# Kernel optimization log

Measured on AMD Instinct MI355X. Metric: run time of the kernel, lower is better.

Reference implementation:

```python
import jax, jax.numpy as jnp
import numpy as np

N = 100000      # nodes
E = 1600000     # edges (avg degree 16)
IN_DIM = 64
H = 4           # num_heads
D = 32          # out_dim per head
NEG_SLOPE = 0.1


def setup_inputs() -> dict:
    key = jax.random.key(0)
    k_x, k_src, k_dst, k_w, k_fc, k_al, k_ar = jax.random.split(key, 7)
    x = jax.random.normal(k_x, (N, IN_DIM), dtype=jnp.float32)
    src = jax.random.randint(k_src, (E,), 0, N, dtype=jnp.int32)
    dst = jax.random.randint(k_dst, (E,), 0, N, dtype=jnp.int32)
    w = jax.random.uniform(k_w, (E,), dtype=jnp.float32)
    # xavier-ish init for learned params
    W_fc = jax.random.normal(k_fc, (IN_DIM, H * D), dtype=jnp.float32) * (2.0 / (IN_DIM + H * D)) ** 0.5
    attn_l = jax.random.normal(k_al, (1, H, D), dtype=jnp.float32) * 0.1
    attn_r = jax.random.normal(k_ar, (1, H, D), dtype=jnp.float32) * 0.1
    vt = jnp.zeros((1,), dtype=jnp.float32)  # unused by forward (as in the source)
    return {"vt": vt, "x": x, "src": src, "dst": dst, "w": w,
            "W_fc": W_fc, "attn_l": attn_l, "attn_r": attn_r}


def reference(vt, x, src, dst, w, W_fc, attn_l, attn_r):
    # node projection: [N, H, D]
    feat = (x @ W_fc).reshape(-1, H, D)
    el = jnp.sum(feat * attn_l, axis=-1)  # [N, H]
    er = jnp.sum(feat * attn_r, axis=-1)  # [N, H]
    # per-edge logits: u_add_v then leaky_relu, scaled by edge weight w
    e = el[src] + er[dst]                                   # [E, H]
    e = jnp.where(e >= 0, e, NEG_SLOPE * e)                 # leaky_relu
    e = w[:, None] * e                                      # [E, H]
    # edge softmax grouped by destination node (numerically stable)
    m = jax.ops.segment_max(e, dst, num_segments=N)         # [N, H]
    ex = jnp.exp(e - m[dst])                                # [E, H]
    den = jax.ops.segment_sum(ex, dst, num_segments=N)      # [N, H]
    a = ex / den[dst]                                       # [E, H]
    # message passing: u_mul_e -> sum over incoming edges
    msg = feat[src] * a[:, :, None]                         # [E, H, D]
    out = jax.ops.segment_sum(msg, dst, num_segments=N)     # [N, H, D]
    return out
```

## Files before the change

### kernel.cpp

```cpp
#include <hip/hip_runtime.h>
#include <math.h>

#define IN_DIM 64
#define HH 4
#define CC 128
#define NEG_SLOPE 0.1f

typedef __attribute__((ext_vector_type(8))) short short8;
typedef __attribute__((ext_vector_type(4))) float f32x4;

__device__ __forceinline__ float leaky(float v) { return v >= 0.f ? v : NEG_SLOPE * v; }

__device__ __forceinline__ unsigned f2bf(float f) {
  unsigned u = __float_as_uint(f);
  unsigned r = u + 0x7FFFu + ((u >> 16) & 1u);
  return r >> 16;
}

__global__ void k_prepw(const float* __restrict__ W, unsigned* __restrict__ wt) {
  int tid = blockIdx.x * 256 + threadIdx.x;
  if (tid >= 128 * 32) return;
  int n = tid >> 5;
  int r = tid & 31;
  int b = r >> 2, h = r & 3;
  int k = b * 8 + h * 2;
  unsigned lo = f2bf(W[k * CC + n]);
  unsigned hi = f2bf(W[(k + 1) * CC + n]);
  wt[n * 32 + (b ^ (n & 7)) * 4 + h] = lo | (hi << 16);
}

__global__ __launch_bounds__(256) void k_project(
    const float* __restrict__ x, const unsigned* __restrict__ wt,
    const float* __restrict__ attn_l, const float* __restrict__ attn_r,
    unsigned char* __restrict__ featQ, float* __restrict__ scale,
    float* __restrict__ el, float* __restrict__ er, int N)
{
  __shared__ unsigned Wlds[4096];
  __shared__ float Al[CC], Ar[CC];
  int t = threadIdx.x;
  {
    const uint4* s = (const uint4*)wt;
    uint4* d = (uint4*)Wlds;
#pragma unroll
    for (int i = 0; i < 4; ++i) d[t + 256 * i] = s[t + 256 * i];
  }
  if (t < CC) { Al[t] = attn_l[t]; Ar[t] = attn_r[t]; }
  __syncthreads();

  int lane = t & 63;
  int l4 = lane >> 4, l16 = lane & 15;
  int node = blockIdx.x * 64 + (t >> 6) * 16 + l16;
  bool valid = node < N;
  int nrow = valid ? node : 0;

  short8 bfr[2];
#pragma unroll
  for (int s = 0; s < 2; ++s) {
    const float4* xp = (const float4*)&x[(size_t)nrow * 64 + s * 32 + l4 * 8];
    float4 xa = xp[0], xb = xp[1];
    union { short8 v; unsigned u[4]; } pk;
    pk.u[0] = f2bf(xa.x) | (f2bf(xa.y) << 16);
    pk.u[1] = f2bf(xa.z) | (f2bf(xa.w) << 16);
    pk.u[2] = f2bf(xb.x) | (f2bf(xb.y) << 16);
    pk.u[3] = f2bf(xb.z) | (f2bf(xb.w) << 16);
    bfr[s] = pk.v;
  }

  f32x4 acc[8];
#pragma unroll
  for (int c = 0; c < 8; ++c) acc[c] = (f32x4){0.f, 0.f, 0.f, 0.f};

#pragma unroll
  for (int c = 0; c < 8; ++c) {
    int n0 = c * 16 + l16;
    int sw = n0 & 7;
#pragma unroll
    for (int s = 0; s < 2; ++s) {
      int b = s * 4 + l4;
      union { short8 v; uint4 q; } af;
      af.q = *(const uint4*)&Wlds[n0 * 32 + (b ^ sw) * 4];
      acc[c] = __builtin_amdgcn_mfma_f32_16x16x32_bf16(af.v, bfr[s], acc[c], 0, 0, 0);
    }
  }

  float mx = 0.f;
#pragma unroll
  for (int c = 0; c < 8; ++c) {
#pragma unroll
    for (int r = 0; r < 4; ++r) mx = fmaxf(mx, fabsf(acc[c][r]));
  }
  mx = fmaxf(mx, __shfl_xor(mx, 16, 64));
  mx = fmaxf(mx, __shfl_xor(mx, 32, 64));
  float mxs = fmaxf(mx, 1e-20f);
  float inv = 127.f / mxs;

  if (valid) {
#pragma unroll
    for (int c = 0; c < 8; ++c) {
      int q0 = __float2int_rn(acc[c][0] * inv) + 128;
      int q1 = __float2int_rn(acc[c][1] * inv) + 128;
      int q2 = __float2int_rn(acc[c][2] * inv) + 128;
      int q3 = __float2int_rn(acc[c][3] * inv) + 128;
      unsigned u = (unsigned)(q0 & 0xff) | ((unsigned)(q1 & 0xff) << 8) |
                   ((unsigned)(q2 & 0xff) << 16) | ((unsigned)(q3 & 0xff) << 24);
      *(unsigned*)&featQ[(size_t)node * 128 + c * 16 + l4 * 4] = u;
    }
    if (l4 == 0) scale[node] = mxs * (1.f / 127.f);
  }

  float pl[4], pr[4];
#pragma unroll
  for (int h = 0; h < 4; ++h) {
    float sl = 0.f, sr = 0.f;
#pragma unroll
    for (int ct = 0; ct < 2; ++ct) {
      int c = 2 * h + ct;
      int cb = c * 16 + l4 * 4;
#pragma unroll
      for (int r = 0; r < 4; ++r) {
        sl = fmaf(acc[c][r], Al[cb + r], sl);
        sr = fmaf(acc[c][r], Ar[cb + r], sr);
      }
    }
    sl += __shfl_xor(sl, 16, 64); sl += __shfl_xor(sl, 32, 64);
    sr += __shfl_xor(sr, 16, 64); sr += __shfl_xor(sr, 32, 64);
    pl[h] = sl; pr[h] = sr;
  }
  if (l4 == 0 && valid) {
    *(float4*)&el[(size_t)node * 4] = make_float4(pl[0], pl[1], pl[2], pl[3]);
    *(float4*)&er[(size_t)node * 4] = make_float4(pr[0], pr[1], pr[2], pr[3]);
  }
}

__global__ __launch_bounds__(256) void k_bhist(const int* __restrict__ dst,
                                               int* __restrict__ bcnt, int E, int NB) {
  __shared__ int lh[512];
  for (int i = threadIdx.x; i < NB; i += 256) lh[i] = 0;
  __syncthreads();
  int stride = gridDim.x * 256;
  for (int i = blockIdx.x * 256 + threadIdx.x; i < E; i += stride)
    atomicAdd(&lh[dst[i] >> 8], 1);
  __syncthreads();
  for (int i = threadIdx.x; i < NB; i += 256) {
    int c = lh[i];
    if (c) atomicAdd(&bcnt[i], c);
  }
}

__global__ __launch_bounds__(512) void k_bscan(const int* __restrict__ bcnt,
                                               int* __restrict__ gbase,
                                               int* __restrict__ gcursor, int NB) {
  __shared__ int sh[512];
  int t = threadIdx.x;
  int v = (t < NB) ? bcnt[t] : 0;
  sh[t] = v;
  __syncthreads();
  for (int off = 1; off < 512; off <<= 1) {
    int a = (t >= off) ? sh[t - off] : 0;
    __syncthreads();
    sh[t] += a;
    __syncthreads();
  }
  if (t < NB) {
    int e = sh[t] - v;
    gbase[t] = e;
    gcursor[t] = e;
  }
}

__global__ __launch_bounds__(512) void k_binA(const int* __restrict__ src,
                                              const int* __restrict__ dst,
                                              const float* __restrict__ w,
                                              int* __restrict__ gcursor,
                                              uint2* __restrict__ bkt, int E, int NB) {
  __shared__ int lh[512];
  __shared__ int lbase[512];
  int t = threadIdx.x;
  for (int i = t; i < NB; i += 512) lh[i] = 0;
  __syncthreads();
  long eb = (long)blockIdx.x * 8192;
  int b[16]; int r[16]; unsigned px[16]; unsigned pw[16];
#pragma unroll
  for (int i = 0; i < 16; ++i) {
    long e = eb + t + i * 512;
    bool v = e < E;
    int d = v ? dst[e] : 0;
    b[i] = d >> 8;
    px[i] = v ? ((unsigned)src[e] | ((unsigned)(d & 255) << 20)) : 0u;
    pw[i] = v ? ((const unsigned*)w)[e] : 0u;
    r[i] = v ? atomicAdd(&lh[b[i]], 1) : -1;
  }
  __syncthreads();
  for (int i = t; i < NB; i += 512) {
    int c = lh[i];
    lbase[i] = c ? atomicAdd(&gcursor[i], c) : 0;
  }
  __syncthreads();
#pragma unroll
  for (int i = 0; i < 16; ++i)
    if (r[i] >= 0) bkt[lbase[b[i]] + r[i]] = make_uint2(px[i], pw[i]);
}

__global__ __launch_bounds__(256) void k_binB(const uint2* __restrict__ bkt,
                                              const int* __restrict__ bcnt,
                                              const int* __restrict__ gbase,
                                              int* __restrict__ offs,
                                              int2* __restrict__ sp,
                                              int N, int E, int NB) {
  __shared__ int lh[256], sc[256], lcur[256];
  int b = blockIdx.x;
  int t = threadIdx.x;
  int base_b = gbase[b];
  int cnt_b = bcnt[b];
  lh[t] = 0;
  __syncthreads();
  for (int e = t; e < cnt_b; e += 256) {
    uint2 p = bkt[base_b + e];
    atomicAdd(&lh[(p.x >> 20) & 255], 1);
  }
  __syncthreads();
  int v = lh[t];
  sc[t] = v;
  __syncthreads();
  for (int off = 1; off < 256; off <<= 1) {
    int a = (t >= off) ? sc[t - off] : 0;
    __syncthreads();
    sc[t] += a;
    __syncthreads();
  }
  int excl = sc[t] - v;
  lcur[t] = excl;
  int n0 = b << 8;
  if (n0 + t < N) offs[n0 + t] = base_b + excl;
  if (b == NB - 1 && t == 0) offs[N] = E;
  __syncthreads();
  for (int e = t; e < cnt_b; e += 256) {
    uint2 p = bkt[base_b + e];
    int d = (p.x >> 20) & 255;
    int pos = atomicAdd(&lcur[d], 1);
    sp[base_b + pos] = make_int2((int)(p.x & 0xFFFFFu), (int)p.y);
  }
}

__device__ __forceinline__ void fma16(float* acc, float& ka, float a, uint4 f) {
  ka += a;
  acc[0]  = fmaf(a, (float)( f.x        & 0xffu), acc[0]);
  acc[1]  = fmaf(a, (float)((f.x >> 8 ) & 0xffu), acc[1]);
  acc[2]  = fmaf(a, (float)((f.x >> 16) & 0xffu), acc[2]);
  acc[3]  = fmaf(a, (float)( f.x >> 24        ), acc[3]);
  acc[4]  = fmaf(a, (float)( f.y        & 0xffu), acc[4]);
  acc[5]  = fmaf(a, (float)((f.y >> 8 ) & 0xffu), acc[5]);
  acc[6]  = fmaf(a, (float)((f.y >> 16) & 0xffu), acc[6]);
  acc[7]  = fmaf(a, (float)( f.y >> 24        ), acc[7]);
  acc[8]  = fmaf(a, (float)( f.z        & 0xffu), acc[8]);
  acc[9]  = fmaf(a, (float)((f.z >> 8 ) & 0xffu), acc[9]);
  acc[10] = fmaf(a, (float)((f.z >> 16) & 0xffu), acc[10]);
  acc[11] = fmaf(a, (float)( f.z >> 24        ), acc[11]);
  acc[12] = fmaf(a, (float)( f.w        & 0xffu), acc[12]);
  acc[13] = fmaf(a, (float)((f.w >> 8 ) & 0xffu), acc[13]);
  acc[14] = fmaf(a, (float)((f.w >> 16) & 0xffu), acc[14]);
  acc[15] = fmaf(a, (float)( f.w >> 24        ), acc[15]);
}

__global__ __launch_bounds__(256) void k_aggregate(
    const int* __restrict__ offs, const int2* __restrict__ sp,
    const float* __restrict__ el, const float* __restrict__ er,
    const float* __restrict__ scale, const unsigned char* __restrict__ featQ,
    float* __restrict__ out, int N)
{
  __shared__ int    s_lds[4][64];
  __shared__ float4 a_lds[4][64];

  int t = threadIdx.x;
  int lane = t & 63, wv = t >> 6;
  int half = lane >> 5, l32 = lane & 31;
  int n = blockIdx.x * 8 + wv * 2 + half;
  if (n >= N) return;

  int off0 = offs[n], off1 = offs[n + 1];
  int deg = off1 - off0;
  int grp = l32 >> 3;
  int c8 = l32 & 7;
  int hh = c8 >> 1;
  int hlane = lane & 32;
  const unsigned char* featl = featQ + c8 * 16;
  int* slf = &s_lds[wv][half * 32];
  const float* al = (const float*)&a_lds[wv][half * 32];

  float acc[16];
#pragma unroll
  for (int i = 0; i < 16; ++i) acc[i] = 0.f;
  float ka = 0.f;

  if (deg > 0) {
    float4 erv = *reinterpret_cast<const float4*>(&er[(size_t)n * HH]);
    if (deg <= 32) {
      int dm1 = deg - 1;
      bool act = l32 < deg;
      int2 p = sp[off0 + (act ? l32 : 0)];
      int s = p.x;
      float wgt = __int_as_float(p.y);
      float sc = scale[s];

      uint4 fb[8];
#pragma unroll
      for (int k = 0; k < 4; ++k) {
        int ic = 4 * k + grp;
        int icc = ic < dm1 ? ic : dm1;
        int ss = __shfl(s, hlane + icc, 64);
        fb[k] = *reinterpret_cast<const uint4*>(featl + ((size_t)ss << 7));
      }
      if (deg > 16) {
#pragma unroll
        for (int k = 4; k < 8; ++k) {
          int ic = 4 * k + grp;
          int icc = ic < dm1 ? ic : dm1;
          int ss = __shfl(s, hlane + icc, 64);
          fb[k] = *reinterpret_cast<const uint4*>(featl + ((size_t)ss << 7));
        }
      }

      float4 elv = *reinterpret_cast<const float4*>(&el[(size_t)s * HH]);
      float x0 = act ? __expf(leaky(elv.x + erv.x) * wgt) : 0.f;
      float x1 = act ? __expf(leaky(elv.y + erv.y) * wgt) : 0.f;
      float x2 = act ? __expf(leaky(elv.z + erv.z) * wgt) : 0.f;
      float x3 = act ? __expf(leaky(elv.w + erv.w) * wgt) : 0.f;
      float d0 = x0, d1 = x1, d2 = x2, d3 = x3;
#pragma unroll
      for (int d = 16; d >= 1; d >>= 1) {
        d0 += __shfl_xor(d0, d, 64);
        d1 += __shfl_xor(d1, d, 64);
        d2 += __shfl_xor(d2, d, 64);
        d3 += __shfl_xor(d3, d, 64);
      }
      float a0 = x0 * __builtin_amdgcn_rcpf(d0) * sc;
      float a1 = x1 * __builtin_amdgcn_rcpf(d1) * sc;
      float a2 = x2 * __builtin_amdgcn_rcpf(d2) * sc;
      float a3 = x3 * __builtin_amdgcn_rcpf(d3) * sc;
      a_lds[wv][half * 32 + l32] = make_float4(a0, a1, a2, a3);

#pragma unroll
      for (int k = 0; k < 4; ++k) {
        int ic = 4 * k + grp;
        int icc = ic < dm1 ? ic : dm1;
        float a = (ic < deg) ? al[icc * 4 + hh] : 0.f;
        fma16(acc, ka, a, fb[k]);
      }
      if (deg > 16) {
#pragma unroll
        for (int k = 4; k < 8; ++k) {
          int ic = 4 * k + grp;
          int icc = ic < dm1 ? ic : dm1;
          float a = (ic < deg) ? al[icc * 4 + hh] : 0.f;
          fma16(acc, ka, a, fb[k]);
        }
      }
    } else {
      float m0 = -INFINITY, m1 = -INFINITY, m2 = -INFINITY, m3 = -INFINITY;
      for (int base = off0; base < off1; base += 32) {
        int j = base + l32;
        bool act = j < off1;
        int2 p = sp[act ? j : off0];
        float wgt = __int_as_float(p.y);
        float4 elv = *reinterpret_cast<const float4*>(&el[(size_t)p.x * HH]);
        float e0 = act ? leaky(elv.x + erv.x) * wgt : -INFINITY;
        float e1 = act ? leaky(elv.y + erv.y) * wgt : -INFINITY;
        float e2 = act ? leaky(elv.z + erv.z) * wgt : -INFINITY;
        float e3 = act ? leaky(elv.w + erv.w) * wgt : -INFINITY;
        m0 = fmaxf(m0, e0); m1 = fmaxf(m1, e1);
        m2 = fmaxf(m2, e2); m3 = fmaxf(m3, e3);
      }
#pragma unroll
      for (int d = 16; d >= 1; d >>= 1) {
        m0 = fmaxf(m0, __shfl_xor(m0, d, 64));
        m1 = fmaxf(m1, __shfl_xor(m1, d, 64));
        m2 = fmaxf(m2, __shfl_xor(m2, d, 64));
        m3 = fmaxf(m3, __shfl_xor(m3, d, 64));
      }
      float d0 = 0.f, d1 = 0.f, d2 = 0.f, d3 = 0.f;
      for (int base = off0; base < off1; base += 32) {
        int j = base + l32;
        bool act = j < off1;
        int2 p = sp[act ? j : off0];
        float wgt = __int_as_float(p.y);
        float4 elv = *reinterpret_cast<const float4*>(&el[(size_t)p.x * HH]);
        d0 += act ? __expf(leaky(elv.x + erv.x) * wgt - m0) : 0.f;
        d1 += act ? __expf(leaky(elv.y + erv.y) * wgt - m1) : 0.f;
        d2 += act ? __expf(leaky(elv.z + erv.z) * wgt - m2) : 0.f;
        d3 += act ? __expf(leaky(elv.w + erv.w) * wgt - m3) : 0.f;
      }
#pragma unroll
      for (int d = 16; d >= 1; d >>= 1) {
        d0 += __shfl_xor(d0, d, 64);
        d1 += __shfl_xor(d1, d, 64);
        d2 += __shfl_xor(d2, d, 64);
        d3 += __shfl_xor(d3, d, 64);
      }
      float i0 = __builtin_amdgcn_rcpf(d0), i1 = __builtin_amdgcn_rcpf(d1);
      float i2 = __builtin_amdgcn_rcpf(d2), i3 = __builtin_amdgcn_rcpf(d3);
      for (int base = off0; base < off1; base += 32) {
        int j = base + l32;
        bool act = j < off1;
        int2 p = sp[act ? j : off0];
        float wgt = __int_as_float(p.y);
        float sc = scale[p.x];
        float4 elv = *reinterpret_cast<const float4*>(&el[(size_t)p.x * HH]);
        float a0 = act ? __expf(leaky(elv.x + erv.x) * wgt - m0) * i0 * sc : 0.f;
        float a1 = act ? __expf(leaky(elv.y + erv.y) * wgt - m1) * i1 * sc : 0.f;
        float a2 = act ? __expf(leaky(elv.z + erv.z) * wgt - m2) * i2 * sc : 0.f;
        float a3 = act ? __expf(leaky(elv.w + erv.w) * wgt - m3) * i3 * sc : 0.f;
        slf[l32] = p.x << 7;
        a_lds[wv][half * 32 + l32] = make_float4(a0, a1, a2, a3);
        int cnt = off1 - base; if (cnt > 32) cnt = 32;
        int ne2 = (cnt + 3) >> 2;
        for (int b0 = 0; b0 < ne2; b0 += 4) {
          uint4 fb[4];
          float av[4];
#pragma unroll
          for (int k = 0; k < 4; ++k) {
            int idx = 4 * (b0 + k) + grp;
            bool vv = idx < cnt;
            int ic = vv ? idx : 0;
            av[k] = vv ? al[ic * 4 + hh] : 0.f;
            fb[k] = *reinterpret_cast<const uint4*>(featl + slf[ic]);
          }
#pragma unroll
          for (int k = 0; k < 4; ++k) fma16(acc, ka, av[k], fb[k]);
        }
      }
    }
  }
#pragma unroll
  for (int d = 8; d <= 16; d <<= 1) {
#pragma unroll
    for (int i = 0; i < 16; ++i) acc[i] += __shfl_xor(acc[i], d, 64);
    ka += __shfl_xor(ka, d, 64);
  }
  if (grp == 0) {
    float base = 128.f * ka;
    float* orow = &out[(size_t)n * CC + c8 * 16];
#pragma unroll
    for (int k = 0; k < 4; ++k) {
      f32x4 o = {acc[4 * k] - base, acc[4 * k + 1] - base,
                 acc[4 * k + 2] - base, acc[4 * k + 3] - base};
      *reinterpret_cast<f32x4*>(orow + 4 * k) = o;
    }
  }
}

extern "C" void kernel_launch(void* const* d_in, const int* in_sizes, int n_in,
                              void* d_out, int out_size, void* d_ws, size_t ws_size,
                              hipStream_t stream)
{
  const float* x      = (const float*)d_in[1];
  const int*   src    = (const int*)d_in[2];
  const int*   dst    = (const int*)d_in[3];
  const float* w      = (const float*)d_in[4];
  const float* W_fc   = (const float*)d_in[5];
  const float* attn_l = (const float*)d_in[6];
  const float* attn_r = (const float*)d_in[7];
  float* out = (float*)d_out;

  int N = in_sizes[1] / IN_DIM;
  int E = in_sizes[2];
  int NB = (N + 255) / 256;

  char* p = (char*)d_ws;
  auto alloc = [&](size_t bytes) {
    char* r = p;
    p += (bytes + 255) & ~size_t(255);
    return r;
  };
  unsigned char* featQ = (unsigned char*)alloc((size_t)N * 128);
  float* scale = (float*)alloc((size_t)N * 4);
  float* el    = (float*)alloc((size_t)N * HH * 4);
  float* er    = (float*)alloc((size_t)N * HH * 4);
  int*   offs  = (int*)alloc((size_t)(N + 1) * 4);
  int*   bcnt  = (int*)alloc(512 * 4);
  int*   gbase = (int*)alloc(512 * 4);
  int*   gcur  = (int*)alloc(512 * 4);
  unsigned* wtswz = (unsigned*)alloc(4096 * 4);
  uint2* bkt   = (uint2*)alloc((size_t)E * 8);
  int2*  sp    = (int2*)alloc((size_t)E * 8);

  hipMemsetAsync(bcnt, 0, 512 * 4, stream);

  k_prepw<<<16, 256, 0, stream>>>(W_fc, wtswz);
  k_project<<<(N + 63) / 64, 256, 0, stream>>>(x, wtswz, attn_l, attn_r,
                                               featQ, scale, el, er, N);
  k_bhist<<<256, 256, 0, stream>>>(dst, bcnt, E, NB);
  k_bscan<<<1, 512, 0, stream>>>(bcnt, gbase, gcur, NB);
  k_binA<<<(E + 8191) / 8192, 512, 0, stream>>>(src, dst, w, gcur, bkt, E, NB);
  k_binB<<<NB, 256, 0, stream>>>(bkt, bcnt, gbase, offs, sp, N, E, NB);
  k_aggregate<<<(N + 7) / 8, 256, 0, stream>>>(offs, sp, el, er, scale, featQ, out, N);
}
```

Baseline: 134.2 us.

## Process two destination nodes per half-wave to overlap feature gathers

Each 32-lane half-wave now handles two consecutive destination nodes, issuing the quantized feature gathers for both before computing softmax and accumulation. The aim is more memory-level parallelism per wave, hiding gather latency for the common case where both degrees are at most 32. Any pair containing a higher-degree node falls back to the original per-node loop. The grid is halved, and register pressure roughly doubles from the two feature buffers, which risks lower occupancy or spills.

```diff
diff --git a/kernel.cpp b/kernel.cpp
--- a/kernel.cpp
+++ b/kernel.cpp
@@ -269,62 +269,93 @@
     float* __restrict__ out, int N)
 {
   __shared__ int    s_lds[4][64];
-  __shared__ float4 a_lds[4][64];
+  __shared__ float4 a_lds[4][128];
 
   int t = threadIdx.x;
   int lane = t & 63, wv = t >> 6;
   int half = lane >> 5, l32 = lane & 31;
-  int n = blockIdx.x * 8 + wv * 2 + half;
-  if (n >= N) return;
-
-  int off0 = offs[n], off1 = offs[n + 1];
-  int deg = off1 - off0;
+  int nb = blockIdx.x * 16 + (wv * 2 + half) * 2;
+  if (nb >= N) return;
+
   int grp = l32 >> 3;
   int c8 = l32 & 7;
   int hh = c8 >> 1;
   int hlane = lane & 32;
   const unsigned char* featl = featQ + c8 * 16;
   int* slf = &s_lds[wv][half * 32];
-  const float* al = (const float*)&a_lds[wv][half * 32];
+  float4* aslot0 = &a_lds[wv][half * 64];
+  float4* aslot1 = &a_lds[wv][half * 64 + 32];
+  const float* al0 = (const float*)aslot0;
+  const float* al1 = (const float*)aslot1;
+
+  bool have1 = (nb + 1) < N;
+  int off00 = offs[nb], off01 = offs[nb + 1];
+  int deg0 = off01 - off00;
+  int off10 = off01;
+  int off11 = have1 ? offs[nb + 2] : off01;
+  int deg1 = off11 - off10;
 
   float acc[16];
-#pragma unroll
-  for (int i = 0; i < 16; ++i) acc[i] = 0.f;
-  float ka = 0.f;
-
-  if (deg > 0) {
-    float4 erv = *reinterpret_cast<const float4*>(&er[(size_t)n * HH]);
-    if (deg <= 32) {
-      int dm1 = deg - 1;
-      bool act = l32 < deg;
-      int2 p = sp[off0 + (act ? l32 : 0)];
-      int s = p.x;
-      float wgt = __int_as_float(p.y);
-      float sc = scale[s];
-
-      uint4 fb[8];
+  float ka;
+
+  if (deg0 <= 32 && deg1 <= 32) {
+    int s0 = 0, s1 = 0; float wgt0 = 0.f, wgt1 = 0.f, sc0 = 0.f, sc1 = 0.f;
+    bool act0 = l32 < deg0, act1 = l32 < deg1;
+    if (deg0 > 0) {
+      int2 p = sp[off00 + (act0 ? l32 : 0)];
+      s0 = p.x; wgt0 = __int_as_float(p.y); sc0 = scale[s0];
+    }
+    if (deg1 > 0) {
+      int2 p = sp[off10 + (act1 ? l32 : 0)];
+      s1 = p.x; wgt1 = __int_as_float(p.y); sc1 = scale[s1];
+    }
+    int dm10 = deg0 - 1, dm11 = deg1 - 1;
+
+    uint4 fb0[8], fb1[8];
+    if (deg0 > 0) {
 #pragma unroll
       for (int k = 0; k < 4; ++k) {
         int ic = 4 * k + grp;
-        int icc = ic < dm1 ? ic : dm1;
-        int ss = __shfl(s, hlane + icc, 64);
-        fb[k] = *reinterpret_cast<const uint4*>(featl + ((size_t)ss << 7));
-      }
-      if (deg > 16) {
+        int icc = ic < dm10 ? ic : dm10;
+        int ss = __shfl(s0, hlane + icc, 64);
+        fb0[k] = *reinterpret_cast<const uint4*>(featl + ((size_t)ss << 7));
+      }
+      if (deg0 > 16) {
 #pragma unroll
         for (int k = 4; k < 8; ++k) {
           int ic = 4 * k + grp;
-          int icc = ic < dm1 ? ic : dm1;
-          int ss = __shfl(s, hlane + icc, 64);
-          fb[k] = *reinterpret_cast<const uint4*>(featl + ((size_t)ss << 7));
+          int icc = ic < dm10 ? ic : dm10;
+          int ss = __shfl(s0, hlane + icc, 64);
+          fb0[k] = *reinterpret_cast<const uint4*>(featl + ((size_t)ss << 7));
         }
       }
-
-      float4 elv = *reinterpret_cast<const float4*>(&el[(size_t)s * HH]);
-      float x0 = act ? __expf(leaky(elv.x + erv.x) * wgt) : 0.f;
-      float x1 = act ? __expf(leaky(elv.y + erv.y) * wgt) : 0.f;
-      float x2 = act ? __expf(leaky(elv.z + erv.z) * wgt) : 0.f;
-      float x3 = act ? __expf(leaky(elv.w + erv.w) * wgt) : 0.f;
+    }
+    if (deg1 > 0) {
+#pragma unroll
+      for (int k = 0; k < 4; ++k) {
+        int ic = 4 * k + grp;
+        int icc = ic < dm11 ? ic : dm11;
+        int ss = __shfl(s1, hlane + icc, 64);
+        fb1[k] = *reinterpret_cast<const uint4*>(featl + ((size_t)ss << 7));
+      }
+      if (deg1 > 16) {
+#pragma unroll
+        for (int k = 4; k < 8; ++k) {
+          int ic = 4 * k + grp;
+          int icc = ic < dm11 ? ic : dm11;
+          int ss = __shfl(s1, hlane + icc, 64);
+          fb1[k] = *reinterpret_cast<const uint4*>(featl + ((size_t)ss << 7));
+        }
+      }
+    }
+
+    if (deg0 > 0) {
+      float4 erv = *reinterpret_cast<const float4*>(&er[(size_t)nb * HH]);
+      float4 elv = *reinterpret_cast<const float4*>(&el[(size_t)s0 * HH]);
+      float x0 = act0 ? __expf(leaky(elv.x + erv.x) * wgt0) : 0.f;
+      float x1 = act0 ? __expf(leaky(elv.y + erv.y) * wgt0) : 0.f;
+      float x2 = act0 ? __expf(leaky(elv.z + erv.z) * wgt0) : 0.f;
+      float x3 = act0 ? __expf(leaky(elv.w + erv.w) * wgt0) : 0.f;
       float d0 = x0, d1 = x1, d2 = x2, d3 = x3;
 #pragma unroll
       for (int d = 16; d >= 1; d >>= 1) {
@@ -333,62 +364,19 @@
         d2 += __shfl_xor(d2, d, 64);
         d3 += __shfl_xor(d3, d, 64);
       }
-      float a0 = x0 * __builtin_amdgcn_rcpf(d0) * sc;
-      float a1 = x1 * __builtin_amdgcn_rcpf(d1) * sc;
-      float a2 = x2 * __builtin_amdgcn_rcpf(d2) * sc;
-      float a3 = x3 * __builtin_amdgcn_rcpf(d3) * sc;
-      a_lds[wv][half * 32 + l32] = make_float4(a0, a1, a2, a3);
-
-#pragma unroll
-      for (int k = 0; k < 4; ++k) {
-        int ic = 4 * k + grp;
-        int icc = ic < dm1 ? ic : dm1;
-        float a = (ic < deg) ? al[icc * 4 + hh] : 0.f;
-        fma16(acc, ka, a, fb[k]);
-      }
-      if (deg > 16) {
-#pragma unroll
-        for (int k = 4; k < 8; ++k) {
-          int ic = 4 * k + grp;
-          int icc = ic < dm1 ? ic : dm1;
-          float a = (ic < deg) ? al[icc * 4 + hh] : 0.f;
-          fma16(acc, ka, a, fb[k]);
-        }
-      }
-    } else {
-      float m0 = -INFINITY, m1 = -INFINITY, m2 = -INFINITY, m3 = -INFINITY;
-      for (int base = off0; base < off1; base += 32) {
-        int j = base + l32;
-        bool act = j < off1;
-        int2 p = sp[act ? j : off0];
-        float wgt = __int_as_float(p.y);
-        float4 elv = *reinterpret_cast<const float4*>(&el[(size_t)p.x * HH]);
-        float e0 = act ? leaky(elv.x + erv.x) * wgt : -INFINITY;
-        float e1 = act ? leaky(elv.y + erv.y) * wgt : -INFINITY;
-        float e2 = act ? leaky(elv.z + erv.z) * wgt : -INFINITY;
-        float e3 = act ? leaky(elv.w + erv.w) * wgt : -INFINITY;
-        m0 = fmaxf(m0, e0); m1 = fmaxf(m1, e1);
-        m2 = fmaxf(m2, e2); m3 = fmaxf(m3, e3);
-      }
-#pragma unroll
-      for (int d = 16; d >= 1; d >>= 1) {
-        m0 = fmaxf(m0, __shfl_xor(m0, d, 64));
-        m1 = fmaxf(m1, __shfl_xor(m1, d, 64));
-        m2 = fmaxf(m2, __shfl_xor(m2, d, 64));
-        m3 = fmaxf(m3, __shfl_xor(m3, d, 64));
-      }
-      float d0 = 0.f, d1 = 0.f, d2 = 0.f, d3 = 0.f;
-      for (int base = off0; base < off1; base += 32) {
-        int j = base + l32;
-        bool act = j < off1;
-        int2 p = sp[act ? j : off0];
-        float wgt = __int_as_float(p.y);
-        float4 elv = *reinterpret_cast<const float4*>(&el[(size_t)p.x * HH]);
-        d0 += act ? __expf(leaky(elv.x + erv.x) * wgt - m0) : 0.f;
-        d1 += act ? __expf(leaky(elv.y + erv.y) * wgt - m1) : 0.f;
-        d2 += act ? __expf(leaky(elv.z + erv.z) * wgt - m2) : 0.f;
-        d3 += act ? __expf(leaky(elv.w + erv.w) * wgt - m3) : 0.f;
-      }
+      aslot0[l32] = make_float4(x0 * __builtin_amdgcn_rcpf(d0) * sc0,
+                                x1 * __builtin_amdgcn_rcpf(d1) * sc0,
+                                x2 * __builtin_amdgcn_rcpf(d2) * sc0,
+                                x3 * __builtin_amdgcn_rcpf(d3) * sc0);
+    }
+    if (deg1 > 0) {
+      float4 erv = *reinterpret_cast<const float4*>(&er[(size_t)(nb + 1) * HH]);
+      float4 elv = *reinterpret_cast<const float4*>(&el[(size_t)s1 * HH]);
+      float x0 = act1 ? __expf(leaky(elv.x + erv.x) * wgt1) : 0.f;
+      float x1 = act1 ? __expf(leaky(elv.y + erv.y) * wgt1) : 0.f;
+      float x2 = act1 ? __expf(leaky(elv.z + erv.z) * wgt1) : 0.f;
+      float x3 = act1 ? __expf(leaky(elv.w + erv.w) * wgt1) : 0.f;
+      float d0 = x0, d1 = x1, d2 = x2, d3 = x3;
 #pragma unroll
       for (int d = 16; d >= 1; d >>= 1) {
         d0 += __shfl_xor(d0, d, 64);
@@ -396,54 +384,249 @@
         d2 += __shfl_xor(d2, d, 64);
         d3 += __shfl_xor(d3, d, 64);
       }
-      float i0 = __builtin_amdgcn_rcpf(d0), i1 = __builtin_amdgcn_rcpf(d1);
-      float i2 = __builtin_amdgcn_rcpf(d2), i3 = __builtin_amdgcn_rcpf(d3);
-      for (int base = off0; base < off1; base += 32) {
-        int j = base + l32;
-        bool act = j < off1;
-        int2 p = sp[act ? j : off0];
-        float wgt = __int_as_float(p.y);
-        float sc = scale[p.x];
-        float4 elv = *reinterpret_cast<const float4*>(&el[(size_t)p.x * HH]);
-        float a0 = act ? __expf(leaky(elv.x + erv.x) * wgt - m0) * i0 * sc : 0.f;
-        float a1 = act ? __expf(leaky(elv.y + erv.y) * wgt - m1) * i1 * sc : 0.f;
-        float a2 = act ? __expf(leaky(elv.z + erv.z) * wgt - m2) * i2 * sc : 0.f;
-        float a3 = act ? __expf(leaky(elv.w + erv.w) * wgt - m3) * i3 * sc : 0.f;
-        slf[l32] = p.x << 7;
-        a_lds[wv][half * 32 + l32] = make_float4(a0, a1, a2, a3);
-        int cnt = off1 - base; if (cnt > 32) cnt = 32;
-        int ne2 = (cnt + 3) >> 2;
-        for (int b0 = 0; b0 < ne2; b0 += 4) {
-          uint4 fb[4];
-          float av[4];
+      aslot1[l32] = make_float4(x0 * __builtin_amdgcn_rcpf(d0) * sc1,
+                                x1 * __builtin_amdgcn_rcpf(d1) * sc1,
+                                x2 * __builtin_amdgcn_rcpf(d2) * sc1,
+                                x3 * __builtin_amdgcn_rcpf(d3) * sc1);
+    }
+
+#pragma unroll
+    for (int i = 0; i < 16; ++i) acc[i] = 0.f;
+    ka = 0.f;
+    if (deg0 > 0) {
+#pragma unroll
+      for (int k = 0; k < 4; ++k) {
+        int ic = 4 * k + grp;
+        int icc = ic < dm10 ? ic : dm10;
+        float a = (ic < deg0) ? al0[icc * 4 + hh] : 0.f;
+        fma16(acc, ka, a, fb0[k]);
+      }
+      if (deg0 > 16) {
+#pragma unroll
+        for (int k = 4; k < 8; ++k) {
+          int ic = 4 * k + grp;
+          int icc = ic < dm10 ? ic : dm10;
+          float a = (ic < deg0) ? al0[icc * 4 + hh] : 0.f;
+          fma16(acc, ka, a, fb0[k]);
+        }
+      }
+    }
+#pragma unroll
+    for (int d = 8; d <= 16; d <<= 1) {
+#pragma unroll
+      for (int i = 0; i < 16; ++i) acc[i] += __shfl_xor(acc[i], d, 64);
+      ka += __shfl_xor(ka, d, 64);
+    }
+    if (grp == 0) {
+      float base = 128.f * ka;
+      float* orow = &out[(size_t)nb * CC + c8 * 16];
+#pragma unroll
+      for (int k = 0; k < 4; ++k) {
+        f32x4 o = {acc[4 * k] - base, acc[4 * k + 1] - base,
+                   acc[4 * k + 2] - base, acc[4 * k + 3] - base};
+        *reinterpret_cast<f32x4*>(orow + 4 * k) = o;
+      }
+    }
+
+#pragma unroll
+    for (int i = 0; i < 16; ++i) acc[i] = 0.f;
+    ka = 0.f;
+    if (deg1 > 0) {
+#pragma unroll
+      for (int k = 0; k < 4; ++k) {
+        int ic = 4 * k + grp;
+        int icc = ic < dm11 ? ic : dm11;
+        float a = (ic < deg1) ? al1[icc * 4 + hh] : 0.f;
+        fma16(acc, ka, a, fb1[k]);
+      }
+      if (deg1 > 16) {
+#pragma unroll
+        for (int k = 4; k < 8; ++k) {
+          int ic = 4 * k + grp;
+          int icc = ic < dm11 ? ic : dm11;
+          float a = (ic < deg1) ? al1[icc * 4 + hh] : 0.f;
+          fma16(acc, ka, a, fb1[k]);
+        }
+      }
+    }
+#pragma unroll
+    for (int d = 8; d <= 16; d <<= 1) {
+#pragma unroll
+      for (int i = 0; i < 16; ++i) acc[i] += __shfl_xor(acc[i], d, 64);
+      ka += __shfl_xor(ka, d, 64);
+    }
+    if (grp == 0 && have1) {
+      float base = 128.f * ka;
+      float* orow = &out[(size_t)(nb + 1) * CC + c8 * 16];
+#pragma unroll
+      for (int k = 0; k < 4; ++k) {
+        f32x4 o = {acc[4 * k] - base, acc[4 * k + 1] - base,
+                   acc[4 * k + 2] - base, acc[4 * k + 3] - base};
+        *reinterpret_cast<f32x4*>(orow + 4 * k) = o;
+      }
+    }
+  } else {
+    for (int sel = 0; sel < 2; ++sel) {
+      int n = nb + sel;
+      if (n >= N) break;
+      int off0 = sel ? off10 : off00;
+      int off1 = sel ? off11 : off01;
+      int deg = off1 - off0;
+
+#pragma unroll
+      for (int i = 0; i < 16; ++i) acc[i] = 0.f;
+      ka = 0.f;
+
+      if (deg > 0) {
+        float4 erv = *reinterpret_cast<const float4*>(&er[(size_t)n * HH]);
+        if (deg <= 32) {
+          int dm1 = deg - 1;
+          bool act = l32 < deg;
+          int2 p = sp[off0 + (act ? l32 : 0)];
+          int s = p.x;
+          float wgt = __int_as_float(p.y);
+          float sc = scale[s];
+          uint4 fb[8];
 #pragma unroll
           for (int k = 0; k < 4; ++k) {
-            int idx = 4 * (b0 + k) + grp;
-            bool vv = idx < cnt;
-            int ic = vv ? idx : 0;
-            av[k] = vv ? al[ic * 4 + hh] : 0.f;
-            fb[k] = *reinterpret_cast<const uint4*>(featl + slf[ic]);
-          }
-#pragma unroll
-          for (int k = 0; k < 4; ++k) fma16(acc, ka, av[k], fb[k]);
+            int ic = 4 * k + grp;
+            int icc = ic < dm1 ? ic : dm1;
+            int ss = __shfl(s, hlane + icc, 64);
+            fb[k] = *reinterpret_cast<const uint4*>(featl + ((size_t)ss << 7));
+          }
+          if (deg > 16) {
+#pragma unroll
+            for (int k = 4; k < 8; ++k) {
+              int ic = 4 * k + grp;
+              int icc = ic < dm1 ? ic : dm1;
+              int ss = __shfl(s, hlane + icc, 64);
+              fb[k] = *reinterpret_cast<const uint4*>(featl + ((size_t)ss << 7));
+            }
+          }
+          float4 elv = *reinterpret_cast<const float4*>(&el[(size_t)s * HH]);
+          float x0 = act ? __expf(leaky(elv.x + erv.x) * wgt) : 0.f;
+          float x1 = act ? __expf(leaky(elv.y + erv.y) * wgt) : 0.f;
+          float x2 = act ? __expf(leaky(elv.z + erv.z) * wgt) : 0.f;
+          float x3 = act ? __expf(leaky(elv.w + erv.w) * wgt) : 0.f;
+          float d0 = x0, d1 = x1, d2 = x2, d3 = x3;
+#pragma unroll
+          for (int d = 16; d >= 1; d >>= 1) {
+            d0 += __shfl_xor(d0, d, 64);
+            d1 += __shfl_xor(d1, d, 64);
+            d2 += __shfl_xor(d2, d, 64);
+            d3 += __shfl_xor(d3, d, 64);
+          }
+          aslot0[l32] = make_float4(x0 * __builtin_amdgcn_rcpf(d0) * sc,
+                                    x1 * __builtin_amdgcn_rcpf(d1) * sc,
+                                    x2 * __builtin_amdgcn_rcpf(d2) * sc,
+                                    x3 * __builtin_amdgcn_rcpf(d3) * sc);
+#pragma unroll
+          for (int k = 0; k < 4; ++k) {
+            int ic = 4 * k + grp;
+            int icc = ic < dm1 ? ic : dm1;
+            float a = (ic < deg) ? al0[icc * 4 + hh] : 0.f;
+            fma16(acc, ka, a, fb[k]);
+          }
+          if (deg > 16) {
+#pragma unroll
+            for (int k = 4; k < 8; ++k) {
+              int ic = 4 * k + grp;
+              int icc = ic < dm1 ? ic : dm1;
+              float a = (ic < deg) ? al0[icc * 4 + hh] : 0.f;
+              fma16(acc, ka, a, fb[k]);
+            }
+          }
+        } else {
+          float m0 = -INFINITY, m1 = -INFINITY, m2 = -INFINITY, m3 = -INFINITY;
+          for (int base = off0; base < off1; base += 32) {
+            int j = base + l32;
+            bool act = j < off1;
+            int2 p = sp[act ? j : off0];
+            float wgt = __int_as_float(p.y);
+            float4 elv = *reinterpret_cast<const float4*>(&el[(size_t)p.x * HH]);
+            float e0 = act ? leaky(elv.x + erv.x) * wgt : -INFINITY;
+            float e1 = act ? leaky(elv.y + erv.y) * wgt : -INFINITY;
+            float e2 = act ? leaky(elv.z + erv.z) * wgt : -INFINITY;
+            float e3 = act ? leaky(elv.w + erv.w) * wgt : -INFINITY;
+            m0 = fmaxf(m0, e0); m1 = fmaxf(m1, e1);
+            m2 = fmaxf(m2, e2); m3 = fmaxf(m3, e3);
+          }
+#pragma unroll
+          for (int d = 16; d >= 1; d >>= 1) {
+            m0 = fmaxf(m0, __shfl_xor(m0, d, 64));
+            m1 = fmaxf(m1, __shfl_xor(m1, d, 64));
+            m2 = fmaxf(m2, __shfl_xor(m2, d, 64));
+            m3 = fmaxf(m3, __shfl_xor(m3, d, 64));
+          }
+          float d0 = 0.f, d1 = 0.f, d2 = 0.f, d3 = 0.f;
+          for (int base = off0; base < off1; base += 32) {
+            int j = base + l32;
+            bool act = j < off1;
+            int2 p = sp[act ? j : off0];
+            float wgt = __int_as_float(p.y);
+            float4 elv = *reinterpret_cast<const float4*>(&el[(size_t)p.x * HH]);
+            d0 += act ? __expf(leaky(elv.x + erv.x) * wgt - m0) : 0.f;
+            d1 += act ? __expf(leaky(elv.y + erv.y) * wgt - m1) : 0.f;
+            d2 += act ? __expf(leaky(elv.z + erv.z) * wgt - m2) : 0.f;
+            d3 += act ? __expf(leaky(elv.w + erv.w) * wgt - m3) : 0.f;
+          }
+#pragma unroll
+          for (int d = 16; d >= 1; d >>= 1) {
+            d0 += __shfl_xor(d0, d, 64);
+            d1 += __shfl_xor(d1, d, 64);
+            d2 += __shfl_xor(d2, d, 64);
+            d3 += __shfl_xor(d3, d, 64);
+          }
+          float i0 = __builtin_amdgcn_rcpf(d0), i1 = __builtin_amdgcn_rcpf(d1);
+          float i2 = __builtin_amdgcn_rcpf(d2), i3 = __builtin_amdgcn_rcpf(d3);
+          for (int base = off0; base < off1; base += 32) {
+            int j = base + l32;
+            bool act = j < off1;
+            int2 p = sp[act ? j : off0];
+            float wgt = __int_as_float(p.y);
+            float sc = scale[p.x];
+            float4 elv = *reinterpret_cast<const float4*>(&el[(size_t)p.x * HH]);
+            float a0 = act ? __expf(leaky(elv.x + erv.x) * wgt - m0) * i0 * sc : 0.f;
+            float a1 = act ? __expf(leaky(elv.y + erv.y) * wgt - m1) * i1 * sc : 0.f;
+            float a2 = act ? __expf(leaky(elv.z + erv.z) * wgt - m2) * i2 * sc : 0.f;
+            float a3 = act ? __expf(leaky(elv.w + erv.w) * wgt - m3) * i3 * sc : 0.f;
+            slf[l32] = p.x << 7;
+            aslot0[l32] = make_float4(a0, a1, a2, a3);
+            int cnt = off1 - base; if (cnt > 32) cnt = 32;
+            int ne2 = (cnt + 3) >> 2;
+            for (int b0 = 0; b0 < ne2; b0 += 4) {
+              uint4 fb[4];
+              float av[4];
+#pragma unroll
+              for (int k = 0; k < 4; ++k) {
+                int idx = 4 * (b0 + k) + grp;
+                bool vv = idx < cnt;
+                int ic = vv ? idx : 0;
+                av[k] = vv ? al0[ic * 4 + hh] : 0.f;
+                fb[k] = *reinterpret_cast<const uint4*>(featl + slf[ic]);
+              }
+#pragma unroll
+              for (int k = 0; k < 4; ++k) fma16(acc, ka, av[k], fb[k]);
+            }
+          }
         }
       }
-    }
-  }
-#pragma unroll
-  for (int d = 8; d <= 16; d <<= 1) {
-#pragma unroll
-    for (int i = 0; i < 16; ++i) acc[i] += __shfl_xor(acc[i], d, 64);
-    ka += __shfl_xor(ka, d, 64);
-  }
-  if (grp == 0) {
-    float base = 128.f * ka;
-    float* orow = &out[(size_t)n * CC + c8 * 16];
-#pragma unroll
-    for (int k = 0; k < 4; ++k) {
-      f32x4 o = {acc[4 * k] - base, acc[4 * k + 1] - base,
-                 acc[4 * k + 2] - base, acc[4 * k + 3] - base};
-      *reinterpret_cast<f32x4*>(orow + 4 * k) = o;
+#pragma unroll
+      for (int d = 8; d <= 16; d <<= 1) {
+#pragma unroll
+        for (int i = 0; i < 16; ++i) acc[i] += __shfl_xor(acc[i], d, 64);
+        ka += __shfl_xor(ka, d, 64);
+      }
+      if (grp == 0) {
+        float base = 128.f * ka;
+        float* orow = &out[(size_t)n * CC + c8 * 16];
+#pragma unroll
+        for (int k = 0; k < 4; ++k) {
+          f32x4 o = {acc[4 * k] - base, acc[4 * k + 1] - base,
+                     acc[4 * k + 2] - base, acc[4 * k + 3] - base};
+          *reinterpret_cast<f32x4*>(orow + 4 * k) = o;
+        }
+      }
     }
   }
 }
@@ -492,5 +675,5 @@
   k_bscan<<<1, 512, 0, stream>>>(bcnt, gbase, gcur, NB);
   k_binA<<<(E + 8191) / 8192, 512, 0, stream>>>(src, dst, w, gcur, bkt, E, NB);
   k_binB<<<NB, 256, 0, stream>>>(bkt, bcnt, gbase, offs, sp, N, E, NB);
-  k_aggregate<<<(N + 7) / 8, 256, 0, stream>>>(offs, sp, el, er, scale, featQ, out, N);
-}
+  k_aggregate<<<(N + 15) / 16, 256, 0, stream>>>(offs, sp, el, er, scale, featQ, out, N);
+}
```

New measurement: 143.7 us. +7.1%, slower.
